# Optimization experiments

Measured on AMD Instinct MI355X. Metric: run time of the kernel, lower is better.

The kernel has to match this reference:

```python
import jax, jax.numpy as jnp
import numpy as np
import math

IN_C = 512
OUT_C = 512
K = 3
STYLE = 512
EPS = 1e-8
MOD_SCALE = 1.0 / math.sqrt(STYLE)        # EqualLinear scale (lr_mul=1)
CONV_SCALE = 1.0 / math.sqrt(IN_C * K * K)  # ModulatedConv2d scale


def setup_inputs() -> dict:
    key = jax.random.key(0)
    k1, k2, k3, k4 = jax.random.split(key, 4)
    return {
        "x": jax.random.normal(k1, (8, IN_C, 64, 64), dtype=jnp.float32),
        "style": jax.random.normal(k2, (8, STYLE), dtype=jnp.float32),
        "mod_weight": jax.random.normal(k3, (IN_C, STYLE), dtype=jnp.float32),
        "mod_bias": jnp.ones((IN_C,), dtype=jnp.float32),
        "weight": jax.random.normal(k4, (1, OUT_C, IN_C, K, K), dtype=jnp.float32),
    }


def _per_sample_conv(xi, wi):
    # xi: [in_c, H, W], wi: [out_c, in_c, K, K]
    out = jax.lax.conv_general_dilated(
        xi[None], wi, window_strides=(1, 1), padding="SAME",
        dimension_numbers=("NCHW", "OIHW", "NCHW"))
    return out[0]


def reference(x, style, mod_weight, mod_bias, weight):
    # EqualLinear modulation: s = style @ (W*scale)^T + bias  -> [B, in_c]
    s = style @ (mod_weight * MOD_SCALE).T + mod_bias
    # per-sample modulated weight: [B, out_c, in_c, K, K]
    w = CONV_SCALE * weight * s[:, None, :, None, None]
    demod = jax.lax.rsqrt(jnp.sum(w * w, axis=(2, 3, 4), keepdims=True) + EPS)
    w = w * demod
    # grouped conv (groups=batch) == vmap of per-sample conv
    out = jax.vmap(_per_sample_conv)(x, w)  # [B, out_c, H, W]
    return out
```

## Files before the change

### kernel.cpp

```cpp
#include <hip/hip_runtime.h>
#include <hip/hip_bf16.h>

typedef __attribute__((ext_vector_type(8))) short bf16x8;
typedef __attribute__((ext_vector_type(16))) float f32x16;
typedef unsigned int u32;

#define MOD_SCALE 0.04419417382415922f
#define CONV_SCALE 0.014731391274719742f

__device__ __forceinline__ unsigned short f2bf(float f) {
  union { float f; u32 u; } v; v.f = f;
  u32 r = v.u + 0x7fffu + ((v.u >> 16) & 1u);
  return (unsigned short)(r >> 16);
}

__device__ __forceinline__ void gload_lds16(const void* g, void* l) {
  __builtin_amdgcn_global_load_lds(
      (const __attribute__((address_space(1))) u32*)g,
      (__attribute__((address_space(3))) u32*)l, 16, 0, 0);
}

__global__ void k_prep(const float* __restrict__ wsrc, ushort* __restrict__ wb,
                       float* __restrict__ wsq, float* __restrict__ zerobuf,
                       const float* __restrict__ style, const float* __restrict__ mw,
                       const float* __restrict__ mb, float* __restrict__ s) {
  __shared__ float wtile[2304];
  const int t = threadIdx.x;
  if (blockIdx.x < 1024) {
    const float4* s4 = (const float4*)(wsrc + (size_t)blockIdx.x * 2304);
    float4* w4 = (float4*)wtile;
    w4[t] = s4[t];
    w4[t + 256] = s4[t + 256];
    if (t < 64) w4[t + 512] = s4[t + 512];
    __syncthreads();
    int idx = blockIdx.x * 256 + t;
    int oc = idx >> 9, ic = idx & 511;
    int icb = ic >> 4, icr = ic & 15;
    if (blockIdx.x == 0 && t < 16) zerobuf[t] = 0.f;
    float sq = 0.f;
    #pragma unroll
    for (int tap = 0; tap < 9; ++tap) {
      float v = wtile[t * 9 + tap];
      sq += v * v;
      wb[((tap * 32 + icb) * 512 + oc) * 16 + icr] = f2bf(v);
    }
    wsq[idx] = sq;
  } else {
    int idx = (blockIdx.x - 1024) * 256 + t;
    int b = idx >> 9, ic = idx & 511;
    const float4* wr = (const float4*)(mw + ic * 512);
    const float4* sr = (const float4*)(style + b * 512);
    float acc = 0.f;
    #pragma unroll 4
    for (int k = 0; k < 128; ++k) {
      float4 a = wr[k], c = sr[k];
      acc += a.x * c.x + a.y * c.y + a.z * c.z + a.w * c.w;
    }
    s[idx] = acc * MOD_SCALE + mb[ic];
  }
}

__global__ void k_pre2(const float* __restrict__ x, const float* __restrict__ s,
                       ushort* __restrict__ xsb, const float* __restrict__ wsq,
                       float* __restrict__ dscale) {
  const int t = threadIdx.x;
  if (blockIdx.x < 512) {
    const int y = blockIdx.x & 63, b = blockIdx.x >> 6;
    const int px = t & 63, icq = t >> 6;
    #pragma unroll
    for (int i = 0; i < 8; ++i) {
      int icb = i * 4 + icq;
      union { ushort u[16]; uint4 v[2]; } pk;
      #pragma unroll
      for (int j = 0; j < 16; ++j) {
        int ic = icb * 16 + j;
        float v = x[(b * 512 + ic) * 4096 + y * 64 + px] * s[b * 512 + ic];
        pk.u[j] = f2bf(v);
      }
      ushort* dst = xsb + ((size_t)((b * 64 + y) * 32 + icb) * 64 + px) * 16;
      *(uint4*)dst = pk.v[0];
      *(uint4*)(dst + 8) = pk.v[1];
    }
  } else {
    int idx = (blockIdx.x - 512) * 256 + t;
    int b = idx >> 9, oc = idx & 511;
    const float4* wq = (const float4*)(wsq + oc * 512);
    const float4* sp = (const float4*)(s + b * 512);
    float acc = 0.f;
    #pragma unroll 4
    for (int k = 0; k < 128; ++k) {
      float4 a = wq[k], c = sp[k];
      acc += a.x * c.x * c.x + a.y * c.y * c.y + a.z * c.z * c.z + a.w * c.w * c.w;
    }
    dscale[idx] = CONV_SCALE * rsqrtf(CONV_SCALE * CONV_SCALE * acc + 1e-8f);
  }
}

#define ABYTES 18432
#define BUFB   39552
#define SMEMSZ (2 * BUFB + 256)
__global__ __launch_bounds__(256, 2) void k_conv(
    const ushort* __restrict__ wb, const ushort* __restrict__ xsb,
    const float* __restrict__ dscale, const float* __restrict__ zerobuf,
    float* __restrict__ out) {
  const int yb = blockIdx.x, ocb = blockIdx.y, b = blockIdx.z;
  const int t = threadIdx.x;
  const int wv = t >> 6, l = t & 63;
  const int lc = l & 31, lh = l >> 5;
  const int wvr = wv >> 1, wvp = wv & 1;
  const int y0 = yb * 8, oc0 = ocb * 64;

  extern __shared__ char smem[];
  float* dss = (float*)(smem + 2 * BUFB);
  if (t < 64) dss[t] = dscale[b * 512 + oc0 + t];

  f32x16 acc[4][2];
  #pragma unroll
  for (int rr = 0; rr < 4; ++rr)
    #pragma unroll
    for (int ocf = 0; ocf < 2; ++ocf)
      #pragma unroll
      for (int k = 0; k < 16; ++k)
        acc[rr][ocf][k] = 0.f;

  const char* asrc[5];
  #pragma unroll
  for (int i = 0; i < 5; ++i) {
    int cid = i * 256 + t;
    int tap = cid >> 7, cc = cid & 127;
    int oc_l = cc >> 1, h = cc & 1;
    asrc[i] = (const char*)wb + (size_t)tap * 524288 + (size_t)(oc0 + oc_l) * 32 + h * 16;
  }
  const char* bsrc[6];
  int bstride[6];
  #pragma unroll
  for (int i = 0; i < 6; ++i) {
    int cid = i * 256 + t;
    int r = cid / 132, rem = cid - r * 132;
    int yy = y0 - 1 + r;
    bool interior = (rem >= 2) && (rem < 130) && ((unsigned)yy < 64u);
    bsrc[i] = interior
        ? (const char*)xsb + (size_t)(b * 64 + yy) * 65536 + (rem - 2) * 16
        : (const char*)zerobuf;
    bstride[i] = interior ? 2048 : 0;
  }

  const int apo = (lc * 2 + lh) * 16;
  const int bco = (wvp * 32 + lc) * 32 + lh * 16;

  auto STAGE = [&](int bo, int icb) {
    char* Ab = smem + bo;
    char* Bb = Ab + ABYTES;
    const int aoff = icb * 16384;
    #pragma unroll
    for (int i = 0; i < 4; ++i)
      gload_lds16(asrc[i] + aoff, Ab + i * 4096 + wv * 1024);
    if (t < 128)
      gload_lds16(asrc[4] + aoff, Ab + 16384 + wv * 1024);
    #pragma unroll
    for (int i = 0; i < 5; ++i)
      gload_lds16(bsrc[i] + icb * bstride[i], Bb + i * 4096 + wv * 1024);
    if (t < 40)
      gload_lds16(bsrc[5] + icb * bstride[5], Bb + 20480);
  };

  auto COMPUTE = [&](int bo) {
    const char* Ab = smem + bo;
    const char* Bb = smem + bo + ABYTES;
    #pragma unroll
    for (int dx = 0; dx < 3; ++dx) {
      bf16x8 bfr[6];
      #pragma unroll
      for (int j = 0; j < 6; ++j)
        bfr[j] = *(const bf16x8*)(Bb + (wvr * 4 + j) * 2112 + dx * 32 + bco);
      bf16x8 af[3][2];
      #pragma unroll
      for (int dy = 0; dy < 3; ++dy)
        #pragma unroll
        for (int ocf = 0; ocf < 2; ++ocf)
          af[dy][ocf] = *(const bf16x8*)(Ab + (dy * 3 + dx) * 2048 + ocf * 1024 + apo);
      #pragma unroll
      for (int dy = 0; dy < 3; ++dy)
        #pragma unroll
        for (int rr = 0; rr < 4; ++rr)
          #pragma unroll
          for (int ocf = 0; ocf < 2; ++ocf)
            acc[rr][ocf] = __builtin_amdgcn_mfma_f32_32x32x16_bf16(
                af[dy][ocf], bfr[rr + dy], acc[rr][ocf], 0, 0, 0);
    }
  };

  STAGE(0, 0);
  __syncthreads();
  if (b & 4) __builtin_amdgcn_s_sleep(73);

  #pragma unroll 1
  for (int it = 0; it < 32; it += 2) {
    STAGE(BUFB, it + 1);
    COMPUTE(0);
    __syncthreads();
    if (it < 30) STAGE(0, it + 2);
    COMPUTE(BUFB);
    __syncthreads();
  }

  #pragma unroll
  for (int rr = 0; rr < 4; ++rr) {
    const int y_row = y0 + wvr * 4 + rr;
    #pragma unroll
    for (int ocf = 0; ocf < 2; ++ocf) {
      #pragma unroll
      for (int reg = 0; reg < 16; ++reg) {
        int oc_l = ocf * 32 + (reg & 3) + 8 * (reg >> 2) + 4 * lh;
        out[(size_t)(b * 512 + oc0 + oc_l) * 4096 + y_row * 64 + wvp * 32 + lc]
            = acc[rr][ocf][reg] * dss[oc_l];
      }
    }
  }
}

extern "C" void kernel_launch(void* const* d_in, const int* in_sizes, int n_in,
                              void* d_out, int out_size, void* d_ws, size_t ws_size,
                              hipStream_t stream) {
  const float* x     = (const float*)d_in[0];
  const float* style = (const float*)d_in[1];
  const float* mw    = (const float*)d_in[2];
  const float* mb    = (const float*)d_in[3];
  const float* wsrc  = (const float*)d_in[4];
  float* out = (float*)d_out;

  char* ws = (char*)d_ws;
  float*  zerobuf = (float*)(ws + 0);
  float*  s       = (float*)(ws + 256);
  float*  dscale  = (float*)(ws + 16640);
  float*  wsq     = (float*)(ws + 33024);
  ushort* wb      = (ushort*)(ws + 1081600);
  ushort* xsb     = (ushort*)(ws + 5800192);

  hipFuncSetAttribute(reinterpret_cast<const void*>(k_conv),
                      hipFuncAttributeMaxDynamicSharedMemorySize, SMEMSZ);

  k_prep<<<dim3(1040), dim3(256), 0, stream>>>(wsrc, wb, wsq, zerobuf, style, mw, mb, s);
  k_pre2<<<dim3(528), dim3(256), 0, stream>>>(x, s, xsb, wsq, dscale);
  k_conv<<<dim3(8, 8, 8), dim3(256), SMEMSZ, stream>>>(wb, xsb, dscale, zerobuf, out);
}
```

Baseline: 181.1 us.

## Enlarge conv tile to 16 rows, triple-buffer input with swizzled LDS

The conv kernel now uses 512 threads per block covering 16 output rows, so each staged weight tile is reused across twice as many pixels. The input halo buffer is triple-buffered with partial vmcnt waits, replacing the double-buffered loop that had two full syncthreads per pair of steps. LDS addressing gets an XOR swizzle to cut bank conflicts, the border columns are zero-filled once, and MFMA sections are raised with setprio. This needs more LDS and registers per block, which may lower occupancy, and the hand-written waitcnt logic is fragile.

```diff
diff --git a/kernel.cpp b/kernel.cpp
--- a/kernel.cpp
+++ b/kernel.cpp
@@ -19,6 +19,8 @@
       (const __attribute__((address_space(1))) u32*)g,
       (__attribute__((address_space(3))) u32*)l, 16, 0, 0);
 }
+
+__device__ __forceinline__ int swz(int c) { return c ^ ((c >> 3) & 7); }
 
 __global__ void k_prep(const float* __restrict__ wsrc, ushort* __restrict__ wb,
                        float* __restrict__ wsq, float* __restrict__ zerobuf,
@@ -96,10 +98,14 @@
   }
 }
 
-#define ABYTES 18432
-#define BUFB   39552
-#define SMEMSZ (2 * BUFB + 256)
-__global__ __launch_bounds__(256, 2) void k_conv(
+#define BROW   2080
+#define ABUF   18432
+#define BBUF   (18 * BROW)
+#define B0OFF  (2 * ABUF)
+#define DSSOFF (B0OFF + 3 * BBUF)
+#define SMEMSZ (DSSOFF + 256)
+
+__global__ __launch_bounds__(512, 2) void k_conv(
     const ushort* __restrict__ wb, const ushort* __restrict__ xsb,
     const float* __restrict__ dscale, const float* __restrict__ zerobuf,
     float* __restrict__ out) {
@@ -108,11 +114,10 @@
   const int wv = t >> 6, l = t & 63;
   const int lc = l & 31, lh = l >> 5;
   const int wvr = wv >> 1, wvp = wv & 1;
-  const int y0 = yb * 8, oc0 = ocb * 64;
+  const int y0 = yb * 16, oc0 = ocb * 64;
 
   extern __shared__ char smem[];
-  float* dss = (float*)(smem + 2 * BUFB);
-  if (t < 64) dss[t] = dscale[b * 512 + oc0 + t];
+  float* dss = (float*)(smem + DSSOFF);
 
   f32x16 acc[4][2];
   #pragma unroll
@@ -123,62 +128,71 @@
       for (int k = 0; k < 16; ++k)
         acc[rr][ocf][k] = 0.f;
 
-  const char* asrc[5];
+  const char* asrc[3];
+  #pragma unroll
+  for (int i = 0; i < 3; ++i) {
+    int cid = (wv + i * 8) * 64 + l;
+    int tap = cid >> 7, pc = cid & 127;
+    int c64 = swz(pc & 63);
+    int oc_l = ((pc >> 6) << 5) + (c64 >> 1), h = c64 & 1;
+    if (tap > 8) tap = 8;
+    asrc[i] = (const char*)wb + (size_t)tap * 524288 + (size_t)(oc0 + oc_l) * 32 + h * 16;
+  }
+  const char* bsrc[5];
+  int bstr[5];
   #pragma unroll
   for (int i = 0; i < 5; ++i) {
-    int cid = i * 256 + t;
-    int tap = cid >> 7, cc = cid & 127;
-    int oc_l = cc >> 1, h = cc & 1;
-    asrc[i] = (const char*)wb + (size_t)tap * 524288 + (size_t)(oc0 + oc_l) * 32 + h * 16;
-  }
-  const char* bsrc[6];
-  int bstride[6];
-  #pragma unroll
-  for (int i = 0; i < 6; ++i) {
-    int cid = i * 256 + t;
-    int r = cid / 132, rem = cid - r * 132;
-    int yy = y0 - 1 + r;
-    bool interior = (rem >= 2) && (rem < 130) && ((unsigned)yy < 64u);
-    bsrc[i] = interior
-        ? (const char*)xsb + (size_t)(b * 64 + yy) * 65536 + (rem - 2) * 16
-        : (const char*)zerobuf;
-    bstride[i] = interior ? 2048 : 0;
-  }
-
-  const int apo = (lc * 2 + lh) * 16;
-  const int bco = (wvp * 32 + lc) * 32 + lh * 16;
-
-  auto STAGE = [&](int bo, int icb) {
-    char* Ab = smem + bo;
-    char* Bb = Ab + ABYTES;
-    const int aoff = icb * 16384;
-    #pragma unroll
-    for (int i = 0; i < 4; ++i)
-      gload_lds16(asrc[i] + aoff, Ab + i * 4096 + wv * 1024);
-    if (t < 128)
-      gload_lds16(asrc[4] + aoff, Ab + 16384 + wv * 1024);
+    int cid = (wv + i * 8) * 64 + l;
+    int r = cid >> 7, pc = cid & 127;
+    int c = swz(pc);
+    int col = c >> 1, h = c & 1;
+    int yy = y0 - 1 + (r < 18 ? r : 17);
+    bool inr = ((unsigned)yy < 64u) && (r < 18);
+    bsrc[i] = inr ? (const char*)xsb + (size_t)(b * 64 + yy) * 65536 + col * 32 + h * 16
+                  : (const char*)zerobuf;
+    bstr[i] = inr ? 2048 : 0;
+  }
+
+  const int apo = swz(lc * 2 + lh) * 16;
+  int boff[3];
+  #pragma unroll
+  for (int dx = 0; dx < 3; ++dx) {
+    int px = wvp * 32 + lc + dx - 1;
+    boff[dx] = ((unsigned)px < 64u) ? swz(px * 2 + lh) * 16 : 2048 + lh * 16;
+  }
+
+  auto STAGE_A = [&](int kA) {
+    char* base = smem + (kA & 1) * ABUF + wv * 1024;
+    const int ko = (kA & 31) * 16384;
+    #pragma unroll
+    for (int i = 0; i < 3; ++i)
+      if (i < 2 || wv < 2)
+        gload_lds16(asrc[i] + ko, base + i * 8192);
+  };
+  auto STAGE_B = [&](int kB, char* bbuf) {
+    const int ko = (kB & 31);
     #pragma unroll
     for (int i = 0; i < 5; ++i)
-      gload_lds16(bsrc[i] + icb * bstride[i], Bb + i * 4096 + wv * 1024);
-    if (t < 40)
-      gload_lds16(bsrc[5] + icb * bstride[5], Bb + 20480);
+      if (i < 4 || wv < 4) {
+        int g = wv + i * 8;
+        gload_lds16(bsrc[i] + ko * bstr[i], bbuf + (g >> 1) * BROW + (g & 1) * 1024);
+      }
   };
 
-  auto COMPUTE = [&](int bo) {
-    const char* Ab = smem + bo;
-    const char* Bb = smem + bo + ABYTES;
+  auto COMPUTE = [&](const char* Ab, const char* Bb) {
     #pragma unroll
     for (int dx = 0; dx < 3; ++dx) {
       bf16x8 bfr[6];
       #pragma unroll
       for (int j = 0; j < 6; ++j)
-        bfr[j] = *(const bf16x8*)(Bb + (wvr * 4 + j) * 2112 + dx * 32 + bco);
+        bfr[j] = *(const bf16x8*)(Bb + (wvr * 4 + j) * BROW + boff[dx]);
       bf16x8 af[3][2];
       #pragma unroll
       for (int dy = 0; dy < 3; ++dy)
         #pragma unroll
         for (int ocf = 0; ocf < 2; ++ocf)
           af[dy][ocf] = *(const bf16x8*)(Ab + (dy * 3 + dx) * 2048 + ocf * 1024 + apo);
+      __builtin_amdgcn_s_setprio(1);
       #pragma unroll
       for (int dy = 0; dy < 3; ++dy)
         #pragma unroll
@@ -187,21 +201,36 @@
           for (int ocf = 0; ocf < 2; ++ocf)
             acc[rr][ocf] = __builtin_amdgcn_mfma_f32_32x32x16_bf16(
                 af[dy][ocf], bfr[rr + dy], acc[rr][ocf], 0, 0, 0);
+      __builtin_amdgcn_s_setprio(0);
     }
   };
 
-  STAGE(0, 0);
-  __syncthreads();
-  if (b & 4) __builtin_amdgcn_s_sleep(73);
-
+  if (t < 64) dss[t] = dscale[b * 512 + oc0 + t];
+  if (t < 108) {
+    int line = t >> 1, q = t & 1;
+    int bi = line / 18, r = line - bi * 18;
+    *(uint4*)(smem + B0OFF + bi * BBUF + r * BROW + 2048 + q * 16) = uint4{0, 0, 0, 0};
+  }
+  STAGE_A(0);
+  STAGE_B(0, smem + B0OFF);
+  STAGE_B(1, smem + B0OFF + BBUF);
+  asm volatile("s_waitcnt lgkmcnt(0)" ::: "memory");
+  asm volatile("s_waitcnt vmcnt(4)");
+  __builtin_amdgcn_s_barrier();
+  __builtin_amdgcn_sched_barrier(0);
+
+  char* bc  = smem + B0OFF;
+  char* bn1 = smem + B0OFF + BBUF;
+  char* bn2 = smem + B0OFF + 2 * BBUF;
   #pragma unroll 1
-  for (int it = 0; it < 32; it += 2) {
-    STAGE(BUFB, it + 1);
-    COMPUTE(0);
-    __syncthreads();
-    if (it < 30) STAGE(0, it + 2);
-    COMPUTE(BUFB);
-    __syncthreads();
+  for (int it = 0; it < 32; ++it) {
+    STAGE_A(it + 1);
+    STAGE_B(it + 2, bn2);
+    COMPUTE(smem + (it & 1) * ABUF, bc);
+    asm volatile("s_waitcnt vmcnt(4)");
+    __builtin_amdgcn_s_barrier();
+    __builtin_amdgcn_sched_barrier(0);
+    char* tmp = bc; bc = bn1; bn1 = bn2; bn2 = tmp;
   }
 
   #pragma unroll
@@ -242,5 +271,5 @@
 
   k_prep<<<dim3(1040), dim3(256), 0, stream>>>(wsrc, wb, wsq, zerobuf, style, mw, mb, s);
   k_pre2<<<dim3(528), dim3(256), 0, stream>>>(x, s, xsb, wsq, dscale);
-  k_conv<<<dim3(8, 8, 8), dim3(256), SMEMSZ, stream>>>(wb, xsb, dscale, zerobuf, out);
-}
+  k_conv<<<dim3(4, 8, 8), dim3(512), SMEMSZ, stream>>>(wb, xsb, dscale, zerobuf, out);
+}
```

Measured after the change: 183.7 us. No clear change (+1.5%).

## Software-pipeline LDS fragment reads against MFMAs with explicit waitcnt scheduling

Applied to the files above, without the earlier changes.

Restructures the conv inner loop so LDS fragment loads for the next dx phase are issued with inline ds_read_b128 while MFMAs for the previous phase run. Manual lgkmcnt waits and sched_barriers pin the order. The A-source pointer array is replaced by one base pointer plus constant offsets, and the staggered s_sleep for half the batches is removed. The goal is to hide LDS latency behind MFMA work and cut register pressure from address arrays. In exchange, the double register buffers raise VGPR use, and the hand-written waitcnt counts must match the real number of outstanding LDS and global-to-LDS operations.

```diff
diff --git a/kernel.cpp b/kernel.cpp
--- a/kernel.cpp
+++ b/kernel.cpp
@@ -99,6 +99,10 @@
 #define ABYTES 18432
 #define BUFB   39552
 #define SMEMSZ (2 * BUFB + 256)
+
+#define DSR(dst, off) asm volatile("ds_read_b128 %0, %1" : "=v"(dst) : "v"(off))
+#define SB0() __builtin_amdgcn_sched_barrier(0)
+
 __global__ __launch_bounds__(256, 2) void k_conv(
     const ushort* __restrict__ wb, const ushort* __restrict__ xsb,
     const float* __restrict__ dscale, const float* __restrict__ zerobuf,
@@ -123,16 +127,11 @@
       for (int k = 0; k < 16; ++k)
         acc[rr][ocf][k] = 0.f;
 
-  const char* asrc[5];
-  #pragma unroll
-  for (int i = 0; i < 5; ++i) {
-    int cid = i * 256 + t;
-    int tap = cid >> 7, cc = cid & 127;
-    int oc_l = cc >> 1, h = cc & 1;
-    asrc[i] = (const char*)wb + (size_t)tap * 524288 + (size_t)(oc0 + oc_l) * 32 + h * 16;
-  }
+  const int th = t >> 7, cc = t & 127;
+  const char* asrc0 = (const char*)wb + (size_t)th * 524288
+                    + (size_t)(oc0 + (cc >> 1)) * 32 + (cc & 1) * 16;
   const char* bsrc[6];
-  int bstride[6];
+  int bstr[6];
   #pragma unroll
   for (int i = 0; i < 6; ++i) {
     int cid = i * 256 + t;
@@ -142,11 +141,14 @@
     bsrc[i] = interior
         ? (const char*)xsb + (size_t)(b * 64 + yy) * 65536 + (rem - 2) * 16
         : (const char*)zerobuf;
-    bstride[i] = interior ? 2048 : 0;
-  }
-
-  const int apo = (lc * 2 + lh) * 16;
-  const int bco = (wvp * 32 + lc) * 32 + lh * 16;
+    bstr[i] = interior ? 2048 : 0;
+  }
+
+  const u32 apo = (u32)((lc * 2 + lh) * 16);
+  u32 brof[6];
+  #pragma unroll
+  for (int j = 0; j < 6; ++j)
+    brof[j] = (u32)(ABYTES + (wvr * 4 + j) * 2112 + (wvp * 32 + lc) * 32 + lh * 16);
 
   auto STAGE = [&](int bo, int icb) {
     char* Ab = smem + bo;
@@ -154,53 +156,62 @@
     const int aoff = icb * 16384;
     #pragma unroll
     for (int i = 0; i < 4; ++i)
-      gload_lds16(asrc[i] + aoff, Ab + i * 4096 + wv * 1024);
+      gload_lds16(asrc0 + (size_t)i * 1048576 + aoff, Ab + i * 4096 + wv * 1024);
     if (t < 128)
-      gload_lds16(asrc[4] + aoff, Ab + 16384 + wv * 1024);
+      gload_lds16(asrc0 + 4 * 1048576 + aoff, Ab + 16384 + wv * 1024);
     #pragma unroll
     for (int i = 0; i < 5; ++i)
-      gload_lds16(bsrc[i] + icb * bstride[i], Bb + i * 4096 + wv * 1024);
+      gload_lds16(bsrc[i] + icb * bstr[i], Bb + i * 4096 + wv * 1024);
     if (t < 40)
-      gload_lds16(bsrc[5] + icb * bstride[5], Bb + 20480);
+      gload_lds16(bsrc[5] + icb * bstr[5], Bb + 20480);
   };
 
-  auto COMPUTE = [&](int bo) {
-    const char* Ab = smem + bo;
-    const char* Bb = smem + bo + ABYTES;
-    #pragma unroll
-    for (int dx = 0; dx < 3; ++dx) {
-      bf16x8 bfr[6];
-      #pragma unroll
-      for (int j = 0; j < 6; ++j)
-        bfr[j] = *(const bf16x8*)(Bb + (wvr * 4 + j) * 2112 + dx * 32 + bco);
-      bf16x8 af[3][2];
-      #pragma unroll
-      for (int dy = 0; dy < 3; ++dy)
-        #pragma unroll
-        for (int ocf = 0; ocf < 2; ++ocf)
-          af[dy][ocf] = *(const bf16x8*)(Ab + (dy * 3 + dx) * 2048 + ocf * 1024 + apo);
-      #pragma unroll
-      for (int dy = 0; dy < 3; ++dy)
-        #pragma unroll
-        for (int rr = 0; rr < 4; ++rr)
-          #pragma unroll
-          for (int ocf = 0; ocf < 2; ++ocf)
-            acc[rr][ocf] = __builtin_amdgcn_mfma_f32_32x32x16_bf16(
-                af[dy][ocf], bfr[rr + dy], acc[rr][ocf], 0, 0, 0);
-    }
-  };
+  #define RPH(bb, aa, dxc, boV)                                                \
+    {                                                                          \
+      _Pragma("unroll")                                                        \
+      for (int j = 0; j < 6; ++j)                                              \
+        DSR(bb[j], (u32)(boV) + brof[j] + (dxc) * 32);                         \
+      _Pragma("unroll")                                                        \
+      for (int dy = 0; dy < 3; ++dy)                                           \
+        _Pragma("unroll")                                                      \
+        for (int ocf = 0; ocf < 2; ++ocf)                                      \
+          DSR(aa[dy][ocf],                                                     \
+              (u32)(boV) + apo + (u32)((dy * 3 + (dxc)) * 2048 + ocf * 1024)); \
+    }
+
+  #define MPH(bb, aa)                                                          \
+    {                                                                          \
+      _Pragma("unroll")                                                        \
+      for (int dy = 0; dy < 3; ++dy)                                           \
+        _Pragma("unroll")                                                      \
+        for (int rr = 0; rr < 4; ++rr)                                         \
+          _Pragma("unroll")                                                    \
+          for (int ocf = 0; ocf < 2; ++ocf)                                    \
+            acc[rr][ocf] = __builtin_amdgcn_mfma_f32_32x32x16_bf16(            \
+                aa[dy][ocf], bb[rr + dy], acc[rr][ocf], 0, 0, 0);              \
+    }
 
   STAGE(0, 0);
   __syncthreads();
-  if (b & 4) __builtin_amdgcn_s_sleep(73);
-
+
+  bf16x8 b0[6], b1[6];
+  bf16x8 a0[3][2], a1[3][2];
   #pragma unroll 1
-  for (int it = 0; it < 32; it += 2) {
-    STAGE(BUFB, it + 1);
-    COMPUTE(0);
-    __syncthreads();
-    if (it < 30) STAGE(0, it + 2);
-    COMPUTE(BUFB);
+  for (int it = 0; it < 32; ++it) {
+    const int bo = (it & 1) * BUFB;
+    if (it < 31) STAGE(BUFB - bo, it + 1);
+    RPH(b0, a0, 0, bo);
+    RPH(b1, a1, 1, bo);
+    asm volatile("s_waitcnt lgkmcnt(12)");
+    SB0();
+    MPH(b0, a0);
+    RPH(b0, a0, 2, bo);
+    asm volatile("s_waitcnt lgkmcnt(12)");
+    SB0();
+    MPH(b1, a1);
+    asm volatile("s_waitcnt lgkmcnt(0)");
+    SB0();
+    MPH(b0, a0);
     __syncthreads();
   }
 
```

Result: slower. 187.9 us (+3.8%).
